# Performance work log

Measured on AMD Instinct MI355X. Metric: run time of the kernel, lower is better.

The kernel has to match this reference:

```python
import jax, jax.numpy as jnp
import numpy as np

B = 131072
GI, GO = 4, 4          # input/output pathway groups
NI, NO = 64, 32        # neurons per input group (256/4), per output group (128/4)


def _gelu(t):
    # torch F.gelu default = exact erf gelu
    return jax.nn.gelu(t, approximate=False)


def setup_inputs() -> dict:
    key = jax.random.key(0)
    ks = jax.random.split(key, 16)
    s = 0.02
    return {
        "x":  jax.random.normal(ks[0], (B, 784), jnp.float32),
        "W1": jax.random.normal(ks[1], (512, 784), jnp.float32) * s,
        "b1": jax.random.normal(ks[2], (512,), jnp.float32) * s,
        "W2": jax.random.normal(ks[3], (256, 512), jnp.float32) * s,
        "b2": jax.random.normal(ks[4], (256,), jnp.float32) * s,
        "W3": jax.random.normal(ks[5], (128, 256), jnp.float32) * s,
        "b3": jax.random.normal(ks[6], (128,), jnp.float32) * s,
        "W4": jax.random.normal(ks[7], (64, 128), jnp.float32) * s,
        "b4": jax.random.normal(ks[8], (64,), jnp.float32) * s,
        "W5": jax.random.normal(ks[9], (32, 64), jnp.float32) * s,
        "b5": jax.random.normal(ks[10], (32,), jnp.float32) * s,
        "W6": jax.random.normal(ks[11], (10, 32), jnp.float32) * s,
        "b6": jax.random.normal(ks[12], (10,), jnp.float32) * s,
        "Wr": jax.random.normal(ks[13], (GI * GO, 256), jnp.float32) * s,
        "br": jax.random.normal(ks[14], (GI * GO,), jnp.float32) * s,
    }


def reference(x, W1, b1, W2, b2, W3, b3, W4, b4, W5, b5, W6, b6, Wr, br):
    # pre-middle dense chain (middle_layer == 3)
    h = _gelu(x @ W1.T + b1)          # [B, 512]
    mid_in = _gelu(h @ W2.T + b2)     # [B, 256]

    # router over 16 pathways; pathway_idx = i*GO + j -> reshape [B, GI, GO]
    pw = jax.nn.softmax(mid_in @ Wr.T + br, axis=-1).reshape(-1, GI, GO)

    # grouped pathway matmuls on fc3 (contiguous neuron groups -> reshape)
    xi = mid_in.reshape(-1, GI, NI)            # [B, GI, NI]
    W3g = W3.reshape(GO, NO, GI, NI)           # [GO, NO, GI, NI]
    part = jnp.einsum('bgi,ongi->bgon', xi, W3g)            # [B, GI, GO, NO]
    part = part + b3.reshape(GO, NO)[None, None]            # bias per pathway
    mid_out = jnp.einsum('bgo,bgon->bon', pw, part).reshape(-1, GO * NO)  # [B,128]
    mid_out = _gelu(mid_out)

    # post-middle dense chain
    h = _gelu(mid_out @ W4.T + b4)    # [B, 64]
    h = _gelu(h @ W5.T + b5)          # [B, 32]
    return h @ W6.T + b6              # [B, 10]
```

## Files before the change

### kernel.cpp

```cpp
#include <hip/hip_runtime.h>
#include <cstdint>

typedef _Float16 f16;
typedef _Float16 f16x4 __attribute__((ext_vector_type(4)));
typedef _Float16 f16x8 __attribute__((ext_vector_type(8)));
typedef float f32x4 __attribute__((ext_vector_type(4)));

#define MFMA16(a, b, c) __builtin_amdgcn_mfma_f32_16x16x32_f16((a), (b), (c), 0, 0, 0)

__device__ __forceinline__ float gelu_f(float x) {
    const float u = x * (1.5957691216f + 0.0713548163f * x * x);
    return x * __builtin_amdgcn_rcpf(1.0f + __expf(-u));
}

__device__ __forceinline__ void load_lds16(const void* g, void* l) {
    __builtin_amdgcn_global_load_lds(
        (const __attribute__((address_space(1))) void*)(uintptr_t)g,
        (__attribute__((address_space(3))) void*)(uint32_t)(uintptr_t)l,
        16, 0, 0);
}

__global__ void k_prep(const float* __restrict__ W1, const float* __restrict__ W2,
                       const float* __restrict__ W3, const float* __restrict__ W4,
                       const float* __restrict__ W5, const float* __restrict__ W6,
                       const float* __restrict__ Wr,
                       f16* __restrict__ W1p, f16* __restrict__ W2f, f16* __restrict__ W3f,
                       f16* __restrict__ W4f, f16* __restrict__ W5f, f16* __restrict__ W6p,
                       f16* __restrict__ Wrf) {
    int i = blockIdx.x * 256 + threadIdx.x;
    if (i < 425984) {
        int r = i / 832, c = i - r * 832;
        W1p[i] = (f16)(c < 784 ? W1[r * 784 + c] : 0.0f);
        return;
    }
    i -= 425984;
    if (i < 131072) { W2f[i] = (f16)W2[i]; return; }
    i -= 131072;
    if (i < 32768) { W3f[i] = (f16)W3[i]; return; }
    i -= 32768;
    if (i < 8192) { W4f[i] = (f16)W4[i]; return; }
    i -= 8192;
    if (i < 2048) { W5f[i] = (f16)W5[i]; return; }
    i -= 2048;
    if (i < 512) {
        int r = i >> 5, c = i & 31;
        W6p[i] = (f16)(r < 10 ? W6[r * 32 + c] : 0.0f);
        return;
    }
    i -= 512;
    if (i < 4096) { Wrf[i] = (f16)Wr[i]; return; }
}

__global__ __launch_bounds__(256, 2)
void k_gemm1(const float* __restrict__ A, const f16* __restrict__ Bw,
             const float* __restrict__ bias, f16* __restrict__ C) {
    __shared__ f16 Bs[2 * 256 * 32];
    const int tid = threadIdx.x;
    const int wave = tid >> 6, lane = tid & 63;
    const int nt = blockIdx.x & 1;
    const size_t mt = blockIdx.x >> 1;
    const size_t row0 = mt * 128;
    const int col0 = nt * 256;
    const int am = lane & 15, akg = lane >> 4, ak = akg * 8;
    const int wm = (wave & 1) * 64, wn = (wave >> 1) * 128;
    const f32x4 zero4 = {0.f, 0.f, 0.f, 0.f};
    const f16x8 zero8 = {0, 0, 0, 0, 0, 0, 0, 0};
    f32x4 acc[4][8];
#pragma unroll
    for (int i = 0; i < 4; ++i)
#pragma unroll
        for (int j = 0; j < 8; ++j) acc[i][j] = zero4;

    const int srow = lane >> 2;
    const int scol = (lane & 3) * 8;

    for (int kt = 0; kt < 13; ++kt) {
        const int kb = kt * 64;
#pragma unroll
        for (int p = 0; p < 2; ++p) {
#pragma unroll
            for (int i = 0; i < 4; ++i) {
                const int inst = wave * 4 + i;
                load_lds16(Bw + (size_t)(col0 + inst * 16 + srow) * 832 + kb + p * 32 + scol,
                           &Bs[p * 8192 + inst * 512]);
            }
        }
        f16x8 af[2][4];
#pragma unroll
        for (int ks = 0; ks < 2; ++ks) {
#pragma unroll
            for (int i = 0; i < 4; ++i) {
                const int c = kb + ks * 32 + ak;
                if (c < 784) {
                    const float* p = A + (row0 + wm + i * 16 + am) * 784 + c;
                    const float4 lo = *(const float4*)p;
                    const float4 hi = *(const float4*)(p + 4);
                    f16x8 v;
                    v[0] = (f16)lo.x; v[1] = (f16)lo.y; v[2] = (f16)lo.z; v[3] = (f16)lo.w;
                    v[4] = (f16)hi.x; v[5] = (f16)hi.y; v[6] = (f16)hi.z; v[7] = (f16)hi.w;
                    af[ks][i] = v;
                } else {
                    af[ks][i] = zero8;
                }
            }
        }
        __syncthreads();
#pragma unroll
        for (int ks = 0; ks < 2; ++ks) {
            f16x8 bf[8];
#pragma unroll
            for (int j = 0; j < 8; ++j)
                bf[j] = *(const f16x8*)&Bs[ks * 8192 + (wn + j * 16 + am) * 32 + ak];
#pragma unroll
            for (int i = 0; i < 4; ++i)
#pragma unroll
                for (int j = 0; j < 8; ++j)
                    acc[i][j] = MFMA16(bf[j], af[ks][i], acc[i][j]);
        }
        __syncthreads();
    }
    const int cc = akg * 4;
#pragma unroll
    for (int i = 0; i < 4; ++i) {
        const size_t row = row0 + wm + i * 16 + am;
#pragma unroll
        for (int j = 0; j < 8; ++j) {
            const int col = col0 + wn + j * 16 + cc;
            const float4 b4 = *(const float4*)(bias + col);
            f16x4 v;
            v[0] = (f16)gelu_f(acc[i][j][0] + b4.x);
            v[1] = (f16)gelu_f(acc[i][j][1] + b4.y);
            v[2] = (f16)gelu_f(acc[i][j][2] + b4.z);
            v[3] = (f16)gelu_f(acc[i][j][3] + b4.w);
            *(f16x4*)(C + row * 512 + col) = v;
        }
    }
}

__global__ __launch_bounds__(256, 2)
void k_gemm2(const f16* __restrict__ A, const f16* __restrict__ Bw,
             const float* __restrict__ bias, f16* __restrict__ C) {
    __shared__ f16 As[2 * 128 * 32];
    __shared__ f16 Bs[2 * 256 * 32];
    const int tid = threadIdx.x;
    const int wave = tid >> 6, lane = tid & 63;
    const size_t row0 = (size_t)blockIdx.x * 128;
    const int am = lane & 15, akg = lane >> 4, ak = akg * 8;
    const int wm = (wave & 1) * 64, wn = (wave >> 1) * 128;
    const f32x4 zero4 = {0.f, 0.f, 0.f, 0.f};
    f32x4 acc[4][8];
#pragma unroll
    for (int i = 0; i < 4; ++i)
#pragma unroll
        for (int j = 0; j < 8; ++j) acc[i][j] = zero4;

    const int srow = lane >> 2;
    const int scol = (lane & 3) * 8;

    for (int kt = 0; kt < 8; ++kt) {
        const int kb = kt * 64;
#pragma unroll
        for (int p = 0; p < 2; ++p) {
#pragma unroll
            for (int i = 0; i < 2; ++i) {
                const int inst = wave * 2 + i;
                load_lds16(A + (row0 + inst * 16 + srow) * 512 + kb + p * 32 + scol,
                           &As[p * 4096 + inst * 512]);
            }
#pragma unroll
            for (int i = 0; i < 4; ++i) {
                const int inst = wave * 4 + i;
                load_lds16(Bw + (size_t)(inst * 16 + srow) * 512 + kb + p * 32 + scol,
                           &Bs[p * 8192 + inst * 512]);
            }
        }
        __syncthreads();
#pragma unroll
        for (int ks = 0; ks < 2; ++ks) {
            f16x8 af[4], bf[8];
#pragma unroll
            for (int i = 0; i < 4; ++i)
                af[i] = *(const f16x8*)&As[ks * 4096 + (wm + i * 16 + am) * 32 + ak];
#pragma unroll
            for (int j = 0; j < 8; ++j)
                bf[j] = *(const f16x8*)&Bs[ks * 8192 + (wn + j * 16 + am) * 32 + ak];
#pragma unroll
            for (int i = 0; i < 4; ++i)
#pragma unroll
                for (int j = 0; j < 8; ++j)
                    acc[i][j] = MFMA16(bf[j], af[i], acc[i][j]);
        }
        __syncthreads();
    }
    const int cc = akg * 4;
#pragma unroll
    for (int i = 0; i < 4; ++i) {
        const size_t row = row0 + wm + i * 16 + am;
#pragma unroll
        for (int j = 0; j < 8; ++j) {
            const int col = wn + j * 16 + cc;
            const float4 b4 = *(const float4*)(bias + col);
            f16x4 v;
            v[0] = (f16)gelu_f(acc[i][j][0] + b4.x);
            v[1] = (f16)gelu_f(acc[i][j][1] + b4.y);
            v[2] = (f16)gelu_f(acc[i][j][2] + b4.z);
            v[3] = (f16)gelu_f(acc[i][j][3] + b4.w);
            *(f16x4*)(C + row * 256 + col) = v;
        }
    }
}

__global__ __launch_bounds__(256, 2)
void k_tail(const f16* __restrict__ MID,
            const f16* __restrict__ W3f, const float* __restrict__ b3,
            const f16* __restrict__ W4f, const float* __restrict__ b4,
            const f16* __restrict__ W5f, const float* __restrict__ b5,
            const f16* __restrict__ W6p, const float* __restrict__ b6v,
            const f16* __restrict__ Wrf, const float* __restrict__ brv,
            float* __restrict__ OUT) {
    __shared__ f16 s_mid[64 * 264];
    __shared__ float s_pw[64 * 20];
    __shared__ f16 s_mo[64 * 136];
    __shared__ f16 s_h4[64 * 72];
    __shared__ f16 s_h5[64 * 40];
    const int tid = threadIdx.x, wave = tid >> 6, lane = tid & 63;
    const size_t r0 = (size_t)blockIdx.x * 64;
    const int am = lane & 15, akg = lane >> 4, ak = akg * 8;
    const int wr = wave * 16;
    const int crow = wr + akg * 4;
    const f32x4 zero4 = {0.f, 0.f, 0.f, 0.f};

    {
        const int row = wr + (lane >> 2), seg = (lane & 3) * 64;
        const f16* src = MID + (r0 + row) * 256 + seg;
        f16* dst = s_mid + row * 264 + seg;
#pragma unroll
        for (int c = 0; c < 8; ++c)
            *(f16x8*)(dst + c * 8) = *(const f16x8*)(src + c * 8);
    }

    {
        f32x4 lacc = zero4;
#pragma unroll
        for (int ks = 0; ks < 8; ++ks) {
            f16x8 a = *(const f16x8*)(s_mid + (wr + am) * 264 + ks * 32 + ak);
            f16x8 b = *(const f16x8*)(Wrf + am * 256 + ks * 32 + ak);
            lacc = MFMA16(a, b, lacc);
        }
        const float brn = brv[am];
#pragma unroll
        for (int r = 0; r < 4; ++r) {
            float l = lacc[r] + brn;
            float mx = l;
#pragma unroll
            for (int m = 1; m <= 8; m <<= 1) mx = fmaxf(mx, __shfl_xor(mx, m));
            const float e = __expf(l - mx);
            float s = e;
#pragma unroll
            for (int m = 1; m <= 8; m <<= 1) s += __shfl_xor(s, m);
            const float p = e / s;
            float sg = p;
            sg += __shfl_xor(sg, 4);
            sg += __shfl_xor(sg, 8);
            s_pw[(crow + r) * 20 + am] = p;
            if (am < 4) s_pw[(crow + r) * 20 + 16 + am] = sg;
        }
    }

    {
        f16x8 a3[4][2];
#pragma unroll
        for (int g = 0; g < 4; ++g)
#pragma unroll
            for (int kh = 0; kh < 2; ++kh)
                a3[g][kh] = *(const f16x8*)(s_mid + (wr + am) * 264 + g * 64 + kh * 32 + ak);
#pragma unroll
        for (int o = 0; o < 4; ++o) {
            float pwv[4][4], sgl[4];
#pragma unroll
            for (int r = 0; r < 4; ++r) {
                sgl[r] = s_pw[(crow + r) * 20 + 16 + o];
#pragma unroll
                for (int g = 0; g < 4; ++g)
                    pwv[g][r] = s_pw[(crow + r) * 20 + g * 4 + o];
            }
#pragma unroll
            for (int ctl = 0; ctl < 2; ++ctl) {
                const int ct = o * 2 + ctl;
                const int col = ct * 16 + am;
                const float bias = b3[col];
                f32x4 oacc;
#pragma unroll
                for (int r = 0; r < 4; ++r) oacc[r] = bias * sgl[r];
#pragma unroll
                for (int g = 0; g < 4; ++g) {
                    f32x4 t = zero4;
                    t = MFMA16(a3[g][0], *(const f16x8*)(W3f + (size_t)col * 256 + g * 64 + ak), t);
                    t = MFMA16(a3[g][1], *(const f16x8*)(W3f + (size_t)col * 256 + g * 64 + 32 + ak), t);
#pragma unroll
                    for (int r = 0; r < 4; ++r) oacc[r] += pwv[g][r] * t[r];
                }
#pragma unroll
                for (int r = 0; r < 4; ++r)
                    s_mo[(crow + r) * 136 + col] = (f16)gelu_f(oacc[r]);
            }
        }
    }

    {
        f16x8 a4[4];
#pragma unroll
        for (int ks = 0; ks < 4; ++ks)
            a4[ks] = *(const f16x8*)(s_mo + (wr + am) * 136 + ks * 32 + ak);
#pragma unroll
        for (int ct = 0; ct < 4; ++ct) {
            const int col = ct * 16 + am;
            f32x4 acc = zero4;
#pragma unroll
            for (int ks = 0; ks < 4; ++ks)
                acc = MFMA16(a4[ks], *(const f16x8*)(W4f + (size_t)col * 128 + ks * 32 + ak), acc);
            const float bias = b4[col];
#pragma unroll
            for (int r = 0; r < 4; ++r)
                s_h4[(crow + r) * 72 + col] = (f16)gelu_f(acc[r] + bias);
        }
    }

    {
        f16x8 a5[2];
#pragma unroll
        for (int ks = 0; ks < 2; ++ks)
            a5[ks] = *(const f16x8*)(s_h4 + (wr + am) * 72 + ks * 32 + ak);
#pragma unroll
        for (int ct = 0; ct < 2; ++ct) {
            const int col = ct * 16 + am;
            f32x4 acc = zero4;
#pragma unroll
            for (int ks = 0; ks < 2; ++ks)
                acc = MFMA16(a5[ks], *(const f16x8*)(W5f + (size_t)col * 64 + ks * 32 + ak), acc);
            const float bias = b5[col];
#pragma unroll
            for (int r = 0; r < 4; ++r)
                s_h5[(crow + r) * 40 + col] = (f16)gelu_f(acc[r] + bias);
        }
    }

    {
        f16x8 a6 = *(const f16x8*)(s_h5 + (wr + am) * 40 + ak);
        f16x8 bw = *(const f16x8*)(W6p + am * 32 + ak);
        f32x4 acc = MFMA16(a6, bw, zero4);
        if (am < 10) {
            const float bb = b6v[am];
#pragma unroll
            for (int r = 0; r < 4; ++r)
                OUT[(r0 + crow + r) * 10 + am] = acc[r] + bb;
        }
    }
}

extern "C" void kernel_launch(void* const* d_in, const int* in_sizes, int n_in,
                              void* d_out, int out_size, void* d_ws, size_t ws_size,
                              hipStream_t stream) {
    const float* x  = (const float*)d_in[0];
    const float* W1 = (const float*)d_in[1];
    const float* b1 = (const float*)d_in[2];
    const float* W2 = (const float*)d_in[3];
    const float* b2 = (const float*)d_in[4];
    const float* W3 = (const float*)d_in[5];
    const float* b3 = (const float*)d_in[6];
    const float* W4 = (const float*)d_in[7];
    const float* b4 = (const float*)d_in[8];
    const float* W5 = (const float*)d_in[9];
    const float* b5 = (const float*)d_in[10];
    const float* W6 = (const float*)d_in[11];
    const float* b6 = (const float*)d_in[12];
    const float* Wr = (const float*)d_in[13];
    const float* br = (const float*)d_in[14];
    float* out = (float*)d_out;

    const int M = in_sizes[0] / 784;

    char* ws = (char*)d_ws;
    f16* W1p = (f16*)ws; ws += 512 * 832 * 2;
    f16* W2f = (f16*)ws; ws += 256 * 512 * 2;
    f16* W3f = (f16*)ws; ws += 128 * 256 * 2;
    f16* W4f = (f16*)ws; ws += 64 * 128 * 2;
    f16* W5f = (f16*)ws; ws += 32 * 64 * 2;
    f16* W6p = (f16*)ws; ws += 16 * 32 * 2;
    f16* Wrf = (f16*)ws; ws += 16 * 256 * 2;
    f16* H1  = (f16*)ws; ws += (size_t)M * 512 * 2;
    f16* MIDB= (f16*)ws; ws += (size_t)M * 256 * 2;

    k_prep<<<2362, 256, 0, stream>>>(W1, W2, W3, W4, W5, W6, Wr,
                                     W1p, W2f, W3f, W4f, W5f, W6p, Wrf);
    k_gemm1<<<(M / 128) * 2, 256, 0, stream>>>(x, W1p, b1, H1);
    k_gemm2<<<M / 128, 256, 0, stream>>>(H1, W2f, b2, MIDB);
    k_tail<<<M / 64, 256, 0, stream>>>(MIDB, W3f, b3, W4f, b4, W5f, b5,
                                       W6p, b6, Wrf, br, out);
}
```

Baseline: 899.0 us.

## Fuse gemm2 with tail and double-buffer swizzled LDS staging in gemm1

The second dense layer is merged with the router, pathway and post-middle chain into a single 512-thread kernel, so the mid activation stays in LDS and is no longer written to and re-read from global memory. gemm1 now stages the fp32 input tile into LDS through global_load_lds with XOR swizzling and double buffering over 32-wide k-steps, instead of issuing direct register loads that convert as they go. gemm2 also gets swizzled double-buffered staging. The fused kernel uses about 138 KB of shared memory, which limits occupancy, and gemm1 now runs twice as many k-iterations, each ending in a barrier.

Result: faster. 817.7 us (-9.0%).

```diff
diff --git a/kernel.cpp b/kernel.cpp
--- a/kernel.cpp
+++ b/kernel.cpp
@@ -54,69 +54,75 @@
 __global__ __launch_bounds__(256, 2)
 void k_gemm1(const float* __restrict__ A, const f16* __restrict__ Bw,
              const float* __restrict__ bias, f16* __restrict__ C) {
-    __shared__ f16 Bs[2 * 256 * 32];
+    __shared__ float As[2][128 * 32];
+    __shared__ f16   Bs[2][256 * 32];
     const int tid = threadIdx.x;
     const int wave = tid >> 6, lane = tid & 63;
     const int nt = blockIdx.x & 1;
     const size_t mt = blockIdx.x >> 1;
     const size_t row0 = mt * 128;
     const int col0 = nt * 256;
-    const int am = lane & 15, akg = lane >> 4, ak = akg * 8;
+    const int am = lane & 15, akg = lane >> 4;
     const int wm = (wave & 1) * 64, wn = (wave >> 1) * 128;
     const f32x4 zero4 = {0.f, 0.f, 0.f, 0.f};
-    const f16x8 zero8 = {0, 0, 0, 0, 0, 0, 0, 0};
     f32x4 acc[4][8];
 #pragma unroll
     for (int i = 0; i < 4; ++i)
 #pragma unroll
         for (int j = 0; j < 8; ++j) acc[i][j] = zero4;
 
-    const int srow = lane >> 2;
-    const int scol = (lane & 3) * 8;
-
-    for (int kt = 0; kt < 13; ++kt) {
-        const int kb = kt * 64;
-#pragma unroll
-        for (int p = 0; p < 2; ++p) {
-#pragma unroll
-            for (int i = 0; i < 4; ++i) {
-                const int inst = wave * 4 + i;
-                load_lds16(Bw + (size_t)(col0 + inst * 16 + srow) * 832 + kb + p * 32 + scol,
-                           &Bs[p * 8192 + inst * 512]);
-            }
-        }
-        f16x8 af[2][4];
-#pragma unroll
-        for (int ks = 0; ks < 2; ++ks) {
-#pragma unroll
-            for (int i = 0; i < 4; ++i) {
-                const int c = kb + ks * 32 + ak;
-                if (c < 784) {
-                    const float* p = A + (row0 + wm + i * 16 + am) * 784 + c;
-                    const float4 lo = *(const float4*)p;
-                    const float4 hi = *(const float4*)(p + 4);
-                    f16x8 v;
-                    v[0] = (f16)lo.x; v[1] = (f16)lo.y; v[2] = (f16)lo.z; v[3] = (f16)lo.w;
-                    v[4] = (f16)hi.x; v[5] = (f16)hi.y; v[6] = (f16)hi.z; v[7] = (f16)hi.w;
-                    af[ks][i] = v;
-                } else {
-                    af[ks][i] = zero8;
-                }
-            }
-        }
-        __syncthreads();
-#pragma unroll
-        for (int ks = 0; ks < 2; ++ks) {
-            f16x8 bf[8];
+    const int arow_l = lane >> 3, aps = lane & 7;
+    const int brow_l = lane >> 2, bps = lane & 3;
+
+    auto stage = [&](int kt, int buf) {
+        const int kb = kt * 32;
+#pragma unroll
+        for (int i = 0; i < 4; ++i) {
+            const int inst = wave * 4 + i;
+            const int row = inst * 8 + arow_l;
+            const int ls = aps ^ (row & 7);
+            int c = kb + ls * 4;
+            if (c > 780) c = 768;
+            load_lds16(A + (row0 + row) * (size_t)784 + c, &As[buf][inst * 256]);
+        }
+#pragma unroll
+        for (int i = 0; i < 4; ++i) {
+            const int inst = wave * 4 + i;
+            const int row = inst * 16 + brow_l;
+            const int ls = bps ^ ((row >> 1) & 3);
+            load_lds16(Bw + (size_t)(col0 + row) * 832 + kb + ls * 8, &Bs[buf][inst * 512]);
+        }
+    };
+
+    stage(0, 0);
+    __syncthreads();
+
+    for (int kt = 0; kt < 26; ++kt) {
+        const int cur = kt & 1;
+        if (kt + 1 < 26) stage(kt + 1, cur ^ 1);
+        f16x8 af[4];
+#pragma unroll
+        for (int i = 0; i < 4; ++i) {
+            const int row = wm + i * 16 + am;
+            const int rx = row & 7;
+            const f32x4 lo = *(const f32x4*)&As[cur][row * 32 + (((akg << 1) ^ rx) << 2)];
+            const f32x4 hi = *(const f32x4*)&As[cur][row * 32 + ((((akg << 1) | 1) ^ rx) << 2)];
+            f16x8 v;
+            v[0] = (f16)lo[0]; v[1] = (f16)lo[1]; v[2] = (f16)lo[2]; v[3] = (f16)lo[3];
+            v[4] = (f16)hi[0]; v[5] = (f16)hi[1]; v[6] = (f16)hi[2]; v[7] = (f16)hi[3];
+            af[i] = v;
+        }
+        f16x8 bf[8];
+#pragma unroll
+        for (int j = 0; j < 8; ++j) {
+            const int row = wn + j * 16 + am;
+            bf[j] = *(const f16x8*)&Bs[cur][row * 32 + ((akg ^ ((row >> 1) & 3)) << 3)];
+        }
+#pragma unroll
+        for (int i = 0; i < 4; ++i)
 #pragma unroll
             for (int j = 0; j < 8; ++j)
-                bf[j] = *(const f16x8*)&Bs[ks * 8192 + (wn + j * 16 + am) * 32 + ak];
-#pragma unroll
-            for (int i = 0; i < 4; ++i)
-#pragma unroll
-                for (int j = 0; j < 8; ++j)
-                    acc[i][j] = MFMA16(bf[j], af[ks][i], acc[i][j]);
-        }
+                acc[i][j] = MFMA16(bf[j], af[i], acc[i][j]);
         __syncthreads();
     }
     const int cc = akg * 4;
@@ -137,107 +143,104 @@
     }
 }
 
-__global__ __launch_bounds__(256, 2)
-void k_gemm2(const f16* __restrict__ A, const f16* __restrict__ Bw,
-             const float* __restrict__ bias, f16* __restrict__ C) {
-    __shared__ f16 As[2 * 128 * 32];
-    __shared__ f16 Bs[2 * 256 * 32];
-    const int tid = threadIdx.x;
-    const int wave = tid >> 6, lane = tid & 63;
+__global__ __launch_bounds__(512, 2)
+void k_mid(const f16* __restrict__ H1v, const f16* __restrict__ W2f,
+           const float* __restrict__ b2,
+           const f16* __restrict__ W3f, const float* __restrict__ b3,
+           const f16* __restrict__ W4f, const float* __restrict__ b4,
+           const f16* __restrict__ W5f, const float* __restrict__ b5,
+           const f16* __restrict__ W6p, const float* __restrict__ b6v,
+           const f16* __restrict__ Wrf, const float* __restrict__ brv,
+           float* __restrict__ OUT) {
+    __shared__ __align__(16) char smem[141312];
+    f16* Am = (f16*)smem;
+    f16* Bm = (f16*)(smem + 32768);
+    f16* s_mid = (f16*)smem;
+    float* s_pw = (float*)(smem + 67584);
+    f16* s_mo = (f16*)(smem + 77824);
+    f16* s_h4 = (f16*)(smem + 112640);
+    f16* s_h5 = (f16*)(smem + 131072);
+    const int tid = threadIdx.x, wave = tid >> 6, lane = tid & 63;
     const size_t row0 = (size_t)blockIdx.x * 128;
     const int am = lane & 15, akg = lane >> 4, ak = akg * 8;
-    const int wm = (wave & 1) * 64, wn = (wave >> 1) * 128;
+    const int wm = (wave & 1) * 64, wn = (wave >> 1) * 64;
     const f32x4 zero4 = {0.f, 0.f, 0.f, 0.f};
-    f32x4 acc[4][8];
+    f32x4 acc[4][4];
 #pragma unroll
     for (int i = 0; i < 4; ++i)
 #pragma unroll
-        for (int j = 0; j < 8; ++j) acc[i][j] = zero4;
-
-    const int srow = lane >> 2;
-    const int scol = (lane & 3) * 8;
-
+        for (int j = 0; j < 4; ++j) acc[i][j] = zero4;
+
+    auto stage = [&](int kt, int buf) {
+        const int kb = kt * 64;
+#pragma unroll
+        for (int t = 0; t < 2; ++t) {
+            const int idx = t * 512 + tid;
+            const int row = idx >> 3;
+            const int ls = (idx & 7) ^ (row & 7);
+            load_lds16(H1v + (row0 + row) * 512 + kb + ls * 8,
+                       Am + buf * 8192 + (t * 512 + wave * 64) * 8);
+        }
+#pragma unroll
+        for (int t = 0; t < 4; ++t) {
+            const int idx = t * 512 + tid;
+            const int row = idx >> 3;
+            const int ls = (idx & 7) ^ (row & 7);
+            load_lds16(W2f + (size_t)row * 512 + kb + ls * 8,
+                       Bm + buf * 16384 + (t * 512 + wave * 64) * 8);
+        }
+    };
+
+    stage(0, 0);
+    __syncthreads();
     for (int kt = 0; kt < 8; ++kt) {
-        const int kb = kt * 64;
-#pragma unroll
-        for (int p = 0; p < 2; ++p) {
-#pragma unroll
-            for (int i = 0; i < 2; ++i) {
-                const int inst = wave * 2 + i;
-                load_lds16(A + (row0 + inst * 16 + srow) * 512 + kb + p * 32 + scol,
-                           &As[p * 4096 + inst * 512]);
+        const int cur = kt & 1;
+        if (kt + 1 < 8) stage(kt + 1, cur ^ 1);
+#pragma unroll
+        for (int ks = 0; ks < 2; ++ks) {
+            f16x8 af[4], bf[4];
+#pragma unroll
+            for (int i = 0; i < 4; ++i) {
+                const int row = wm + i * 16 + am;
+                af[i] = *(const f16x8*)&Am[cur * 8192 + row * 64 +
+                                           ((((ks << 2) | akg) ^ (row & 7)) << 3)];
             }
 #pragma unroll
-            for (int i = 0; i < 4; ++i) {
-                const int inst = wave * 4 + i;
-                load_lds16(Bw + (size_t)(inst * 16 + srow) * 512 + kb + p * 32 + scol,
-                           &Bs[p * 8192 + inst * 512]);
+            for (int j = 0; j < 4; ++j) {
+                const int row = wn + j * 16 + am;
+                bf[j] = *(const f16x8*)&Bm[cur * 16384 + row * 64 +
+                                           ((((ks << 2) | akg) ^ (row & 7)) << 3)];
             }
+#pragma unroll
+            for (int i = 0; i < 4; ++i)
+#pragma unroll
+                for (int j = 0; j < 4; ++j)
+                    acc[i][j] = MFMA16(bf[j], af[i], acc[i][j]);
         }
         __syncthreads();
-#pragma unroll
-        for (int ks = 0; ks < 2; ++ks) {
-            f16x8 af[4], bf[8];
-#pragma unroll
-            for (int i = 0; i < 4; ++i)
-                af[i] = *(const f16x8*)&As[ks * 4096 + (wm + i * 16 + am) * 32 + ak];
-#pragma unroll
-            for (int j = 0; j < 8; ++j)
-                bf[j] = *(const f16x8*)&Bs[ks * 8192 + (wn + j * 16 + am) * 32 + ak];
-#pragma unroll
-            for (int i = 0; i < 4; ++i)
-#pragma unroll
-                for (int j = 0; j < 8; ++j)
-                    acc[i][j] = MFMA16(bf[j], af[i], acc[i][j]);
-        }
-        __syncthreads();
-    }
-    const int cc = akg * 4;
-#pragma unroll
-    for (int i = 0; i < 4; ++i) {
-        const size_t row = row0 + wm + i * 16 + am;
-#pragma unroll
-        for (int j = 0; j < 8; ++j) {
-            const int col = wn + j * 16 + cc;
-            const float4 b4 = *(const float4*)(bias + col);
-            f16x4 v;
-            v[0] = (f16)gelu_f(acc[i][j][0] + b4.x);
-            v[1] = (f16)gelu_f(acc[i][j][1] + b4.y);
-            v[2] = (f16)gelu_f(acc[i][j][2] + b4.z);
-            v[3] = (f16)gelu_f(acc[i][j][3] + b4.w);
-            *(f16x4*)(C + row * 256 + col) = v;
-        }
-    }
-}
-
-__global__ __launch_bounds__(256, 2)
-void k_tail(const f16* __restrict__ MID,
-            const f16* __restrict__ W3f, const float* __restrict__ b3,
-            const f16* __restrict__ W4f, const float* __restrict__ b4,
-            const f16* __restrict__ W5f, const float* __restrict__ b5,
-            const f16* __restrict__ W6p, const float* __restrict__ b6v,
-            const f16* __restrict__ Wrf, const float* __restrict__ brv,
-            float* __restrict__ OUT) {
-    __shared__ f16 s_mid[64 * 264];
-    __shared__ float s_pw[64 * 20];
-    __shared__ f16 s_mo[64 * 136];
-    __shared__ f16 s_h4[64 * 72];
-    __shared__ f16 s_h5[64 * 40];
-    const int tid = threadIdx.x, wave = tid >> 6, lane = tid & 63;
-    const size_t r0 = (size_t)blockIdx.x * 64;
-    const int am = lane & 15, akg = lane >> 4, ak = akg * 8;
+    }
+    {
+        const int cc = akg * 4;
+#pragma unroll
+        for (int i = 0; i < 4; ++i) {
+            const int row = wm + i * 16 + am;
+#pragma unroll
+            for (int j = 0; j < 4; ++j) {
+                const int col = wn + j * 16 + cc;
+                const float4 bb = *(const float4*)(b2 + col);
+                f16x4 v;
+                v[0] = (f16)gelu_f(acc[i][j][0] + bb.x);
+                v[1] = (f16)gelu_f(acc[i][j][1] + bb.y);
+                v[2] = (f16)gelu_f(acc[i][j][2] + bb.z);
+                v[3] = (f16)gelu_f(acc[i][j][3] + bb.w);
+                *(f16x4*)&s_mid[row * 264 + col] = v;
+            }
+        }
+    }
+    __syncthreads();
+
     const int wr = wave * 16;
     const int crow = wr + akg * 4;
-    const f32x4 zero4 = {0.f, 0.f, 0.f, 0.f};
-
-    {
-        const int row = wr + (lane >> 2), seg = (lane & 3) * 64;
-        const f16* src = MID + (r0 + row) * 256 + seg;
-        f16* dst = s_mid + row * 264 + seg;
-#pragma unroll
-        for (int c = 0; c < 8; ++c)
-            *(f16x8*)(dst + c * 8) = *(const f16x8*)(src + c * 8);
-    }
 
     {
         f32x4 lacc = zero4;
@@ -315,14 +318,14 @@
 #pragma unroll
         for (int ct = 0; ct < 4; ++ct) {
             const int col = ct * 16 + am;
-            f32x4 acc = zero4;
+            f32x4 acc4 = zero4;
 #pragma unroll
             for (int ks = 0; ks < 4; ++ks)
-                acc = MFMA16(a4[ks], *(const f16x8*)(W4f + (size_t)col * 128 + ks * 32 + ak), acc);
+                acc4 = MFMA16(a4[ks], *(const f16x8*)(W4f + (size_t)col * 128 + ks * 32 + ak), acc4);
             const float bias = b4[col];
 #pragma unroll
             for (int r = 0; r < 4; ++r)
-                s_h4[(crow + r) * 72 + col] = (f16)gelu_f(acc[r] + bias);
+                s_h4[(crow + r) * 72 + col] = (f16)gelu_f(acc4[r] + bias);
         }
     }
 
@@ -334,26 +337,26 @@
 #pragma unroll
         for (int ct = 0; ct < 2; ++ct) {
             const int col = ct * 16 + am;
-            f32x4 acc = zero4;
+            f32x4 acc5 = zero4;
 #pragma unroll
             for (int ks = 0; ks < 2; ++ks)
-                acc = MFMA16(a5[ks], *(const f16x8*)(W5f + (size_t)col * 64 + ks * 32 + ak), acc);
+                acc5 = MFMA16(a5[ks], *(const f16x8*)(W5f + (size_t)col * 64 + ks * 32 + ak), acc5);
             const float bias = b5[col];
 #pragma unroll
             for (int r = 0; r < 4; ++r)
-                s_h5[(crow + r) * 40 + col] = (f16)gelu_f(acc[r] + bias);
+                s_h5[(crow + r) * 40 + col] = (f16)gelu_f(acc5[r] + bias);
         }
     }
 
     {
         f16x8 a6 = *(const f16x8*)(s_h5 + (wr + am) * 40 + ak);
         f16x8 bw = *(const f16x8*)(W6p + am * 32 + ak);
-        f32x4 acc = MFMA16(a6, bw, zero4);
+        f32x4 acc6 = MFMA16(a6, bw, zero4);
         if (am < 10) {
             const float bb = b6v[am];
 #pragma unroll
             for (int r = 0; r < 4; ++r)
-                OUT[(r0 + crow + r) * 10 + am] = acc[r] + bb;
+                OUT[(row0 + crow + r) * 10 + am] = acc6[r] + bb;
         }
     }
 }
@@ -389,12 +392,10 @@
     f16* W6p = (f16*)ws; ws += 16 * 32 * 2;
     f16* Wrf = (f16*)ws; ws += 16 * 256 * 2;
     f16* H1  = (f16*)ws; ws += (size_t)M * 512 * 2;
-    f16* MIDB= (f16*)ws; ws += (size_t)M * 256 * 2;
 
     k_prep<<<2362, 256, 0, stream>>>(W1, W2, W3, W4, W5, W6, Wr,
                                      W1p, W2f, W3f, W4f, W5f, W6p, Wrf);
     k_gemm1<<<(M / 128) * 2, 256, 0, stream>>>(x, W1p, b1, H1);
-    k_gemm2<<<M / 128, 256, 0, stream>>>(H1, W2f, b2, MIDB);
-    k_tail<<<M / 64, 256, 0, stream>>>(MIDB, W3f, b3, W4f, b4, W5f, b5,
+    k_mid<<<M / 128, 512, 0, stream>>>(H1, W2f, b2, W3f, b3, W4f, b4, W5f, b5,
                                        W6p, b6, Wrf, br, out);
 }
```
